# Optimization experiments

Measured on AMD Instinct MI355X. Metric: run time of the kernel, lower is better.

Reference implementation:

```python
import jax, jax.numpy as jnp
import numpy as np

P_FACTOR = 3.0
EPS = 1e-12  # F.normalize eps


def _l2norm(x):
    n = jnp.sqrt(jnp.sum(x * x, axis=-1, keepdims=True))
    return x / jnp.maximum(n, EPS)


def setup_inputs() -> dict:
    key = jax.random.key(0)
    ks = jax.random.split(key, 7)
    B, N, F, E = 4096, 16384, 768, 512
    X = jax.random.normal(ks[0], (B, F), dtype=jnp.float32)
    D = jax.random.normal(ks[1], (N, F), dtype=jnp.float32)
    r = jax.random.uniform(ks[2], (N, 1), dtype=jnp.float32)
    g_w = jax.random.normal(ks[3], (E, F), dtype=jnp.float32) * (1.0 / np.sqrt(F))
    g_b = jax.random.normal(ks[4], (E,), dtype=jnp.float32) * 0.01
    h_w = jax.random.normal(ks[5], (1, 1), dtype=jnp.float32)
    h_b = jax.random.normal(ks[6], (1,), dtype=jnp.float32) * 0.01
    return {"X": X, "D": D, "r": r, "g_w": g_w, "g_b": g_b, "h_w": h_w, "h_b": h_b}


def reference(X, D, r, g_w, g_b, h_w, h_b):
    # r in {0..1} -> {-1..1}
    r2 = r * 2.0 - 1.0
    # feature embedding g applied to both queries and exemplars
    Xe = X @ g_w.T + g_b            # [B, E]
    De = D @ g_w.T + g_b            # [N, E]
    # cosine similarity
    a = _l2norm(Xe) @ _l2norm(De).T  # [B, N]
    # power-law sign activation: |a|^p * sign(a)
    a = jnp.power(jnp.abs(a), P_FACTOR) * jnp.sign(a)
    # weighted exemplar sum (echo)
    echo = a @ r2                    # [B, 1]
    # class embedding h (Linear 1 -> 1)
    logits = echo @ h_w.T + h_b      # [B, 1]
    preds = jax.nn.sigmoid(logits)
    return (logits, preds)
```

## Files before the change

kernel.cpp:

```cpp
#include <hip/hip_runtime.h>
#include <hip/hip_bf16.h>
#include <hip/hip_fp8.h>
#include <stdint.h>

#define P_B 4096
#define P_N 16384
#define P_F 768
#define P_E 512
#define NKT_F 24
#define NKTP_E 8
#define CPAD 776
#define EPAD 136

typedef __attribute__((ext_vector_type(8))) __bf16 bf16x8;
typedef __attribute__((ext_vector_type(4))) float f32x4;

__device__ __forceinline__ unsigned short bfbits(float x) {
    __bf16 h = (__bf16)x;
    union { __bf16 h; unsigned short u; } cv;
    cv.h = h;
    return cv.u;
}
__device__ __forceinline__ float bf2f(unsigned short u) {
    union { float f; unsigned int i; } cv;
    cv.i = ((unsigned int)u) << 16;
    return cv.f;
}
__device__ __forceinline__ unsigned char f8bits(float x) {
    __hip_fp8_e4m3 h(x);
    return (unsigned char)h.__x;
}


__global__ __launch_bounds__(256) void convert_pack_kernel(
    const float* __restrict__ X, const float* __restrict__ D,
    const float* __restrict__ gw,
    unsigned short* __restrict__ xdpk, unsigned short* __restrict__ gwpk,
    float* __restrict__ zbase)
{
    __shared__ unsigned short T[16 * CPAD];
    const int tid = threadIdx.x;
    const int rb = blockIdx.x;

    if (rb < 97) {
        const int z = rb * 256 + tid;
        if (z < P_B + P_N + P_B) zbase[z] = 0.0f;
    }

    const float* src;
    unsigned short* dstbase;
    if (rb < 256)       { src = X  + (size_t)rb * 16 * P_F;          dstbase = xdpk + (size_t)rb * NKT_F * 512; }
    else if (rb < 1280) { src = D  + (size_t)(rb - 256) * 16 * P_F;  dstbase = xdpk + (size_t)rb * NKT_F * 512; }
    else                { src = gw + (size_t)(rb - 1280) * 16 * P_F; dstbase = gwpk + (size_t)(rb - 1280) * NKT_F * 512; }

#pragma unroll
    for (int it = 0; it < 12; ++it) {
        const int flat = it * 1024 + tid * 4;
        const int row = flat / P_F;
        const int col = flat - row * P_F;
        const float4 v = *(const float4*)(src + (size_t)row * P_F + col);
        unsigned short* t = &T[row * CPAD + col];
        t[0] = bfbits(v.x); t[1] = bfbits(v.y); t[2] = bfbits(v.z); t[3] = bfbits(v.w);
    }
    __syncthreads();

#pragma unroll
    for (int it = 0; it < 6; ++it) {
        const int m = it * 256 + tid;
        const int kt = m >> 6;
        const int lane = m & 63;
        const int r = lane & 15;
        const int k = kt * 32 + (lane >> 4) * 8;
        const uint4 frag = *(const uint4*)(&T[r * CPAD + k]);
        *(uint4*)(dstbase + (size_t)(kt * 64 + lane) * 8) = frag;
    }
}

__global__ __launch_bounds__(256, 2) void embed_pk_kernel(
    const unsigned short* __restrict__ xdpk, const unsigned short* __restrict__ gwpk,
    const float* __restrict__ gb,
    unsigned char* __restrict__ embpk8, float* __restrict__ norm2)
{
    __shared__ unsigned short Es[128 * EPAD];
    const int tid = threadIdx.x, lane = tid & 63, wave = tid >> 6;
    const int q = lane >> 4, c = lane & 15;
    const int colTile = blockIdx.x;
    const int rowTile = blockIdx.y;
    const int rbA0 = rowTile * 8 + (wave >> 1) * 4;
    const int rbB0 = colTile * 8 + (wave & 1) * 4;

    const unsigned short* pa[4];
    const unsigned short* pb[4];
#pragma unroll
    for (int i = 0; i < 4; i++)
        pa[i] = xdpk + ((size_t)(rbA0 + i) * NKT_F * 64 + lane) * 8;
#pragma unroll
    for (int j = 0; j < 4; j++)
        pb[j] = gwpk + ((size_t)(rbB0 + j) * NKT_F * 64 + lane) * 8;

    f32x4 acc[4][4];
    const f32x4 zero = {0.f, 0.f, 0.f, 0.f};
#pragma unroll
    for (int i = 0; i < 4; i++)
#pragma unroll
        for (int j = 0; j < 4; j++) acc[i][j] = zero;

#pragma unroll
    for (int kt = 0; kt < NKT_F; ++kt) {
        bf16x8 af[4], bfr[4];
#pragma unroll
        for (int i = 0; i < 4; i++) af[i] = *(const bf16x8*)(pa[i] + (size_t)kt * 512);
#pragma unroll
        for (int j = 0; j < 4; j++) bfr[j] = *(const bf16x8*)(pb[j] + (size_t)kt * 512);
#pragma unroll
        for (int i = 0; i < 4; i++)
#pragma unroll
            for (int j = 0; j < 4; j++)
                acc[i][j] = __builtin_amdgcn_mfma_f32_16x16x32_bf16(af[i], bfr[j], acc[i][j], 0, 0, 0);
    }

    float ss[4][4];
#pragma unroll
    for (int i = 0; i < 4; i++)
#pragma unroll
        for (int r = 0; r < 4; r++) ss[i][r] = 0.f;
#pragma unroll
    for (int j = 0; j < 4; j++) {
        const int lcbase = (wave & 1) * 64 + j * 16 + c;
        const float bias = gb[colTile * 128 + lcbase];
#pragma unroll
        for (int i = 0; i < 4; i++) {
#pragma unroll
            for (int r = 0; r < 4; r++) {
                const int lr = (wave >> 1) * 64 + i * 16 + q * 4 + r;
                const float v = acc[i][j][r] + bias;
                const unsigned short hb = bfbits(v);
                Es[lr * EPAD + lcbase] = hb;
                const float vs = bf2f(hb);
                ss[i][r] = fmaf(vs, vs, ss[i][r]);
            }
        }
    }
#pragma unroll
    for (int i = 0; i < 4; i++)
#pragma unroll
        for (int r = 0; r < 4; r++) {
            float s = ss[i][r];
            s += __shfl_xor(s, 1);
            s += __shfl_xor(s, 2);
            s += __shfl_xor(s, 4);
            s += __shfl_xor(s, 8);
            ss[i][r] = s;
        }
    if (c == 0) {
#pragma unroll
        for (int i = 0; i < 4; i++)
#pragma unroll
            for (int r = 0; r < 4; r++) {
                const int rowg = rowTile * 128 + (wave >> 1) * 64 + i * 16 + q * 4 + r;
                atomicAdd(&norm2[rowg], ss[i][r]);
            }
    }
    __syncthreads();

#pragma unroll
    for (int it = 0; it < 4; ++it) {
        const int m = it * 256 + tid;
        const int rbl = m >> 7;
        const int rest = m & 127;
        const int ktpl = rest >> 6;
        const int lane2 = rest & 63;
        const int r2 = lane2 & 15;
        const int q2 = lane2 >> 4;
        const int lr = rbl * 16 + r2;
        const unsigned short* e0 = &Es[lr * EPAD + ktpl * 64 + q2 * 8];
        const unsigned short* e1 = e0 + 32;
        union { unsigned char b[16]; uint4 v; } outw;
#pragma unroll
        for (int t = 0; t < 8; t++) outw.b[t]     = f8bits(bf2f(e0[t]));
#pragma unroll
        for (int t = 0; t < 8; t++) outw.b[8 + t] = f8bits(bf2f(e1[t]));
        const size_t rb = (size_t)(rowTile * 8 + rbl);
        const size_t ktp = (size_t)(colTile * 2 + ktpl);
        *(uint4*)(embpk8 + ((rb * NKTP_E + ktp) * 64 + lane2) * 16) = outw.v;
    }
}

__global__ void finalize_kernel(float* __restrict__ nf, const float* __restrict__ r)
{
    const int i = blockIdx.x * 256 + threadIdx.x;
    if (i >= P_B + P_N) return;
    float nrm = sqrtf(nf[i]);
    nrm = fmaxf(nrm, 1e-12f);
    const float inv = 1.0f / nrm;
    float w = inv * inv * inv;
    if (i >= P_B) {
        const float rv = r[i - P_B];
        w *= (2.0f * rv - 1.0f);
    }
    nf[i] = w;
}

__global__ __launch_bounds__(256, 2) void echo_pk_kernel(
    const unsigned char* __restrict__ embpk8, const float* __restrict__ fbuf,
    float* __restrict__ echo)
{
    const int tid = threadIdx.x, lane = tid & 63, wave = tid >> 6;
    const int q = lane >> 4, c = lane & 15;
    const int bid = blockIdx.x;
    const int sb = bid >> 6, w = bid & 63;
    const int btile = (sb & 3) * 8 + (w & 7);
    const int ntile = (sb >> 2) * 8 + (w >> 3);
    const int row0 = btile * 128;
    const int col0 = ntile * 128;
    const int rbA0 = btile * 8 + (wave >> 1) * 4;
    const int rbB0 = 256 + ntile * 8 + (wave & 1) * 4;

    const unsigned char* pa[4];
    const unsigned char* pb[4];
#pragma unroll
    for (int i = 0; i < 4; i++)
        pa[i] = embpk8 + ((size_t)(rbA0 + i) * NKTP_E * 64 + lane) * 16;
#pragma unroll
    for (int j = 0; j < 4; j++)
        pb[j] = embpk8 + ((size_t)(rbB0 + j) * NKTP_E * 64 + lane) * 16;

    f32x4 acc[4][4];
    const f32x4 zero = {0.f, 0.f, 0.f, 0.f};
#pragma unroll
    for (int i = 0; i < 4; i++)
#pragma unroll
        for (int j = 0; j < 4; j++) acc[i][j] = zero;

#pragma unroll
    for (int ktp = 0; ktp < NKTP_E; ++ktp) {
        union { uint4 v; long l[2]; } ua[4], ub[4];
#pragma unroll
        for (int i = 0; i < 4; i++) ua[i].v = *(const uint4*)(pa[i] + (size_t)ktp * 1024);
#pragma unroll
        for (int j = 0; j < 4; j++) ub[j].v = *(const uint4*)(pb[j] + (size_t)ktp * 1024);
        __builtin_amdgcn_s_setprio(1);
#pragma unroll
        for (int h = 0; h < 2; h++)
#pragma unroll
            for (int i = 0; i < 4; i++)
#pragma unroll
                for (int j = 0; j < 4; j++)
                    acc[i][j] = __builtin_amdgcn_mfma_f32_16x16x32_fp8_fp8(
                        ua[i].l[h], ub[j].l[h], acc[i][j], 0, 0, 0);
        __builtin_amdgcn_s_setprio(0);
    }

    const float* fX = fbuf;
    const float* fD = fbuf + P_B;
    float wc[4];
#pragma unroll
    for (int j = 0; j < 4; j++) wc[j] = fD[col0 + (wave & 1) * 64 + j * 16 + c];
    float p[4][4];
#pragma unroll
    for (int i = 0; i < 4; i++)
#pragma unroll
        for (int r = 0; r < 4; r++) p[i][r] = 0.f;
#pragma unroll
    for (int i = 0; i < 4; i++)
#pragma unroll
        for (int j = 0; j < 4; j++)
#pragma unroll
            for (int r = 0; r < 4; r++) {
                const float v = acc[i][j][r];
                const float v3 = v * v * v;
                p[i][r] = fmaf(v3, wc[j], p[i][r]);
            }
#pragma unroll
    for (int i = 0; i < 4; i++)
#pragma unroll
        for (int r = 0; r < 4; r++) {
            float s = p[i][r];
            s += __shfl_xor(s, 1);
            s += __shfl_xor(s, 2);
            s += __shfl_xor(s, 4);
            s += __shfl_xor(s, 8);
            p[i][r] = s;
        }
    if (c == 0) {
#pragma unroll
        for (int i = 0; i < 4; i++)
#pragma unroll
            for (int r = 0; r < 4; r++) {
                const int rowg = row0 + (wave >> 1) * 64 + i * 16 + q * 4 + r;
                atomicAdd(&echo[rowg], p[i][r] * fX[rowg]);
            }
    }
}

__global__ void head_kernel(const float* __restrict__ echo, const float* __restrict__ hw,
                            const float* __restrict__ hb, float* __restrict__ out)
{
    const int i = blockIdx.x * 256 + threadIdx.x;
    if (i >= P_B) return;
    const float logit = fmaf(echo[i], hw[0], hb[0]);
    out[i] = logit;
    out[P_B + i] = 1.0f / (1.0f + expf(-logit));
}

extern "C" void kernel_launch(void* const* d_in, const int* in_sizes, int n_in,
                              void* d_out, int out_size, void* d_ws, size_t ws_size,
                              hipStream_t stream)
{
    const float* X  = (const float*)d_in[0];
    const float* D  = (const float*)d_in[1];
    const float* r  = (const float*)d_in[2];
    const float* gw = (const float*)d_in[3];
    const float* gb = (const float*)d_in[4];
    const float* hw = (const float*)d_in[5];
    const float* hb = (const float*)d_in[6];
    float* out = (float*)d_out;

    char* ws = (char*)d_ws;
    const size_t xdpk_bytes   = (size_t)1280 * NKT_F * 64 * 8 * 2;
    const size_t gwpk_bytes   = (size_t)32 * NKT_F * 64 * 8 * 2;
    const size_t embpk8_bytes = (size_t)1280 * NKTP_E * 64 * 16;

    unsigned short* xdpk   = (unsigned short*)ws;
    unsigned short* gwpk   = (unsigned short*)(ws + xdpk_bytes);
    unsigned char*  embpk8 = (unsigned char*)(ws + xdpk_bytes + gwpk_bytes);
    float* norm2 = (float*)(ws + xdpk_bytes + gwpk_bytes + embpk8_bytes);
    float* echo = norm2 + (P_B + P_N);

    convert_pack_kernel<<<dim3(1312), 256, 0, stream>>>(X, D, gw, xdpk, gwpk, norm2);
    embed_pk_kernel<<<dim3(4, 160), 256, 0, stream>>>(xdpk, gwpk, gb, embpk8, norm2);
    finalize_kernel<<<dim3((P_B + P_N + 255) / 256), 256, 0, stream>>>(norm2, r);
    echo_pk_kernel<<<dim3(4096), 256, 0, stream>>>(embpk8, norm2, echo);
    head_kernel<<<dim3((P_B + 255) / 256), 256, 0, stream>>>(echo, hw, hb, out);
}
```

Baseline: 192.2 us.

## Fuse X/D bf16 conversion into embedding GEMM via LDS-staged A tile

The separate pass that converted X and D to packed bf16 in a global workspace is removed. The embedding kernel now loads 32 fp32 rows straight into LDS as bf16 and computes all 512 embedding columns per block, so each block owns full rows and still does the fp8 pack and norm accumulation. This drops a full write and re-read of the converted inputs. In exchange gw fragments are re-read by every block, LDS per block grows, and MFMA issue is raised with setprio.

```diff
diff --git a/kernel.cpp b/kernel.cpp
--- a/kernel.cpp
+++ b/kernel.cpp
@@ -10,7 +10,7 @@
 #define NKT_F 24
 #define NKTP_E 8
 #define CPAD 776
-#define EPAD 136
+#define EPAD3 520
 
 typedef __attribute__((ext_vector_type(8))) __bf16 bf16x8;
 typedef __attribute__((ext_vector_type(4))) float f32x4;
@@ -33,25 +33,19 @@
 
 
 __global__ __launch_bounds__(256) void convert_pack_kernel(
-    const float* __restrict__ X, const float* __restrict__ D,
-    const float* __restrict__ gw,
-    unsigned short* __restrict__ xdpk, unsigned short* __restrict__ gwpk,
+    const float* __restrict__ gw, unsigned short* __restrict__ gwpk,
     float* __restrict__ zbase)
 {
     __shared__ unsigned short T[16 * CPAD];
     const int tid = threadIdx.x;
     const int rb = blockIdx.x;
 
-    if (rb < 97) {
-        const int z = rb * 256 + tid;
-        if (z < P_B + P_N + P_B) zbase[z] = 0.0f;
-    }
-
-    const float* src;
-    unsigned short* dstbase;
-    if (rb < 256)       { src = X  + (size_t)rb * 16 * P_F;          dstbase = xdpk + (size_t)rb * NKT_F * 512; }
-    else if (rb < 1280) { src = D  + (size_t)(rb - 256) * 16 * P_F;  dstbase = xdpk + (size_t)rb * NKT_F * 512; }
-    else                { src = gw + (size_t)(rb - 1280) * 16 * P_F; dstbase = gwpk + (size_t)(rb - 1280) * NKT_F * 512; }
+    const int z = rb * 256 + tid;
+    if (z < P_B + P_N + P_B) zbase[z] = 0.0f;
+    if (rb >= 32) return;
+
+    const float* src = gw + (size_t)rb * 16 * P_F;
+    unsigned short* dstbase = gwpk + (size_t)rb * NKT_F * 512;
 
 #pragma unroll
     for (int it = 0; it < 12; ++it) {
@@ -77,72 +71,86 @@
 }
 
 __global__ __launch_bounds__(256, 2) void embed_pk_kernel(
-    const unsigned short* __restrict__ xdpk, const unsigned short* __restrict__ gwpk,
-    const float* __restrict__ gb,
+    const float* __restrict__ X, const float* __restrict__ D,
+    const unsigned short* __restrict__ gwpk, const float* __restrict__ gb,
     unsigned char* __restrict__ embpk8, float* __restrict__ norm2)
 {
-    __shared__ unsigned short Es[128 * EPAD];
+    __shared__ union {
+        unsigned short T[32 * CPAD];
+        unsigned short Es[32 * EPAD3];
+    } sh;
     const int tid = threadIdx.x, lane = tid & 63, wave = tid >> 6;
     const int q = lane >> 4, c = lane & 15;
-    const int colTile = blockIdx.x;
-    const int rowTile = blockIdx.y;
-    const int rbA0 = rowTile * 8 + (wave >> 1) * 4;
-    const int rbB0 = colTile * 8 + (wave & 1) * 4;
-
-    const unsigned short* pa[4];
-    const unsigned short* pb[4];
-#pragma unroll
-    for (int i = 0; i < 4; i++)
-        pa[i] = xdpk + ((size_t)(rbA0 + i) * NKT_F * 64 + lane) * 8;
-#pragma unroll
-    for (int j = 0; j < 4; j++)
-        pb[j] = gwpk + ((size_t)(rbB0 + j) * NKT_F * 64 + lane) * 8;
-
-    f32x4 acc[4][4];
+    const int rowTile = blockIdx.x;
+    const float* src = (rowTile < 128) ? (X + (size_t)rowTile * 32 * P_F)
+                                       : (D + (size_t)(rowTile - 128) * 32 * P_F);
+
+#pragma unroll
+    for (int it = 0; it < 24; ++it) {
+        const int flat = it * 1024 + tid * 4;
+        const int row = flat / P_F;
+        const int col = flat - row * P_F;
+        const float4 v = *(const float4*)(src + (size_t)row * P_F + col);
+        unsigned short* t = &sh.T[row * CPAD + col];
+        t[0] = bfbits(v.x); t[1] = bfbits(v.y); t[2] = bfbits(v.z); t[3] = bfbits(v.w);
+    }
+    __syncthreads();
+
+    const unsigned short* pb[8];
+#pragma unroll
+    for (int j = 0; j < 8; j++)
+        pb[j] = gwpk + ((size_t)(wave * 8 + j) * NKT_F * 64 + lane) * 8;
+
+    f32x4 acc[2][8];
     const f32x4 zero = {0.f, 0.f, 0.f, 0.f};
 #pragma unroll
-    for (int i = 0; i < 4; i++)
-#pragma unroll
-        for (int j = 0; j < 4; j++) acc[i][j] = zero;
+    for (int i = 0; i < 2; i++)
+#pragma unroll
+        for (int j = 0; j < 8; j++) acc[i][j] = zero;
 
 #pragma unroll
     for (int kt = 0; kt < NKT_F; ++kt) {
-        bf16x8 af[4], bfr[4];
-#pragma unroll
-        for (int i = 0; i < 4; i++) af[i] = *(const bf16x8*)(pa[i] + (size_t)kt * 512);
-#pragma unroll
-        for (int j = 0; j < 4; j++) bfr[j] = *(const bf16x8*)(pb[j] + (size_t)kt * 512);
-#pragma unroll
-        for (int i = 0; i < 4; i++)
-#pragma unroll
-            for (int j = 0; j < 4; j++)
+        bf16x8 af[2], bfr[8];
+#pragma unroll
+        for (int i = 0; i < 2; i++)
+            af[i] = *(const bf16x8*)(&sh.T[(i * 16 + (lane & 15)) * CPAD
+                                           + kt * 32 + (lane >> 4) * 8]);
+#pragma unroll
+        for (int j = 0; j < 8; j++) bfr[j] = *(const bf16x8*)(pb[j] + (size_t)kt * 512);
+        __builtin_amdgcn_s_setprio(1);
+#pragma unroll
+        for (int i = 0; i < 2; i++)
+#pragma unroll
+            for (int j = 0; j < 8; j++)
                 acc[i][j] = __builtin_amdgcn_mfma_f32_16x16x32_bf16(af[i], bfr[j], acc[i][j], 0, 0, 0);
-    }
-
-    float ss[4][4];
-#pragma unroll
-    for (int i = 0; i < 4; i++)
+        __builtin_amdgcn_s_setprio(0);
+    }
+    __syncthreads();
+
+    float ss[2][4];
+#pragma unroll
+    for (int i = 0; i < 2; i++)
 #pragma unroll
         for (int r = 0; r < 4; r++) ss[i][r] = 0.f;
 #pragma unroll
-    for (int j = 0; j < 4; j++) {
-        const int lcbase = (wave & 1) * 64 + j * 16 + c;
-        const float bias = gb[colTile * 128 + lcbase];
-#pragma unroll
-        for (int i = 0; i < 4; i++) {
+    for (int j = 0; j < 8; j++) {
+        const int lc = wave * 128 + j * 16 + c;
+        const float bias = gb[lc];
+#pragma unroll
+        for (int i = 0; i < 2; i++) {
 #pragma unroll
             for (int r = 0; r < 4; r++) {
-                const int lr = (wave >> 1) * 64 + i * 16 + q * 4 + r;
+                const int lr = i * 16 + q * 4 + r;
                 const float v = acc[i][j][r] + bias;
                 const unsigned short hb = bfbits(v);
-                Es[lr * EPAD + lcbase] = hb;
+                sh.Es[lr * EPAD3 + lc] = hb;
                 const float vs = bf2f(hb);
                 ss[i][r] = fmaf(vs, vs, ss[i][r]);
             }
         }
     }
 #pragma unroll
-    for (int i = 0; i < 4; i++)
+    for (int i = 0; i < 2; i++)
 #pragma unroll
         for (int r = 0; r < 4; r++) {
             float s = ss[i][r];
@@ -154,10 +162,10 @@
         }
     if (c == 0) {
 #pragma unroll
-        for (int i = 0; i < 4; i++)
+        for (int i = 0; i < 2; i++)
 #pragma unroll
             for (int r = 0; r < 4; r++) {
-                const int rowg = rowTile * 128 + (wave >> 1) * 64 + i * 16 + q * 4 + r;
+                const int rowg = rowTile * 32 + i * 16 + q * 4 + r;
                 atomicAdd(&norm2[rowg], ss[i][r]);
             }
     }
@@ -166,23 +174,22 @@
 #pragma unroll
     for (int it = 0; it < 4; ++it) {
         const int m = it * 256 + tid;
-        const int rbl = m >> 7;
-        const int rest = m & 127;
+        const int rbl = m >> 9;
+        const int rest = m & 511;
         const int ktpl = rest >> 6;
         const int lane2 = rest & 63;
         const int r2 = lane2 & 15;
         const int q2 = lane2 >> 4;
         const int lr = rbl * 16 + r2;
-        const unsigned short* e0 = &Es[lr * EPAD + ktpl * 64 + q2 * 8];
+        const unsigned short* e0 = &sh.Es[lr * EPAD3 + ktpl * 64 + q2 * 8];
         const unsigned short* e1 = e0 + 32;
         union { unsigned char b[16]; uint4 v; } outw;
 #pragma unroll
         for (int t = 0; t < 8; t++) outw.b[t]     = f8bits(bf2f(e0[t]));
 #pragma unroll
         for (int t = 0; t < 8; t++) outw.b[8 + t] = f8bits(bf2f(e1[t]));
-        const size_t rb = (size_t)(rowTile * 8 + rbl);
-        const size_t ktp = (size_t)(colTile * 2 + ktpl);
-        *(uint4*)(embpk8 + ((rb * NKTP_E + ktp) * 64 + lane2) * 16) = outw.v;
+        const size_t rb = (size_t)(rowTile * 2 + rbl);
+        *(uint4*)(embpk8 + ((rb * NKTP_E + (size_t)ktpl) * 64 + lane2) * 16) = outw.v;
     }
 }
 
@@ -317,18 +324,16 @@
     float* out = (float*)d_out;
 
     char* ws = (char*)d_ws;
-    const size_t xdpk_bytes   = (size_t)1280 * NKT_F * 64 * 8 * 2;
     const size_t gwpk_bytes   = (size_t)32 * NKT_F * 64 * 8 * 2;
     const size_t embpk8_bytes = (size_t)1280 * NKTP_E * 64 * 16;
 
-    unsigned short* xdpk   = (unsigned short*)ws;
-    unsigned short* gwpk   = (unsigned short*)(ws + xdpk_bytes);
-    unsigned char*  embpk8 = (unsigned char*)(ws + xdpk_bytes + gwpk_bytes);
-    float* norm2 = (float*)(ws + xdpk_bytes + gwpk_bytes + embpk8_bytes);
+    unsigned short* gwpk   = (unsigned short*)ws;
+    unsigned char*  embpk8 = (unsigned char*)(ws + gwpk_bytes);
+    float* norm2 = (float*)(ws + gwpk_bytes + embpk8_bytes);
     float* echo = norm2 + (P_B + P_N);
 
-    convert_pack_kernel<<<dim3(1312), 256, 0, stream>>>(X, D, gw, xdpk, gwpk, norm2);
-    embed_pk_kernel<<<dim3(4, 160), 256, 0, stream>>>(xdpk, gwpk, gb, embpk8, norm2);
+    convert_pack_kernel<<<dim3(97), 256, 0, stream>>>(gw, gwpk, norm2);
+    embed_pk_kernel<<<dim3(640), 256, 0, stream>>>(X, D, gwpk, gb, embpk8, norm2);
     finalize_kernel<<<dim3((P_B + P_N + 255) / 256), 256, 0, stream>>>(norm2, r);
     echo_pk_kernel<<<dim3(4096), 256, 0, stream>>>(embpk8, norm2, echo);
     head_kernel<<<dim3((P_B + 255) / 256), 256, 0, stream>>>(echo, hw, hb, out);
```

New measurement: 181.6 us. -5.5%, faster.
